# Performance work log

Measured on AMD Instinct MI355X. Metric: run time of the kernel, lower is better.

## Reference

```python
import jax, jax.numpy as jnp
import numpy as np

DIM = 1024
NUM_HEADS = 16
HEAD_DIM = DIM // NUM_HEADS
SCALE = HEAD_DIM ** -0.5


def rotate_half(x):
    x1, x2 = jnp.split(x, 2, axis=-1)
    return jnp.concatenate((-x2, x1), axis=-1)


def setup_inputs() -> dict:
    key = jax.random.key(0)
    ks = jax.random.split(key, 8)
    B, N = 2, 2048
    x = jax.random.normal(ks[0], (B, N, DIM), dtype=jnp.float32)
    # RoPE tables, broadcast over batch and heads
    pos = jnp.arange(N, dtype=jnp.float32)[:, None]
    inv_freq = 1.0 / (10000.0 ** (jnp.arange(0, HEAD_DIM, 2, dtype=jnp.float32) / HEAD_DIM))
    ang = pos * inv_freq[None, :]                       # [N, HEAD_DIM/2]
    ang = jnp.concatenate([ang, ang], axis=-1)          # [N, HEAD_DIM]
    rope_cos = jnp.cos(ang)[None, None]                 # [1,1,N,HEAD_DIM]
    rope_sin = jnp.sin(ang)[None, None]
    s = DIM ** -0.5
    qkv_w = jax.random.normal(ks[1], (3 * DIM, DIM), dtype=jnp.float32) * s
    qkv_b = jnp.zeros((3 * DIM,), dtype=jnp.float32)
    proj_w = jax.random.normal(ks[2], (DIM, DIM), dtype=jnp.float32) * s
    proj_b = jnp.zeros((DIM,), dtype=jnp.float32)
    return {"x": x, "rope_cos": rope_cos, "rope_sin": rope_sin,
            "qkv_w": qkv_w, "qkv_b": qkv_b, "proj_w": proj_w, "proj_b": proj_b}


def reference(x, rope_cos, rope_sin, qkv_w, qkv_b, proj_w, proj_b):
    B, N, C = x.shape
    H, D = NUM_HEADS, HEAD_DIM
    qkv = x @ qkv_w.T + qkv_b                            # [B,N,3C]
    qkv = qkv.reshape(B, N, 3, H, D).transpose(2, 0, 3, 1, 4)  # [3,B,H,N,D]
    q, k, v = qkv[0], qkv[1], qkv[2]
    # RoPE on q, k
    q = q * rope_cos + rotate_half(q) * rope_sin
    k = k * rope_cos + rotate_half(k) * rope_sin
    # scaled dot-product attention
    scores = jnp.einsum('bhnd,bhmd->bhnm', q, k) * SCALE
    attn = jax.nn.softmax(scores, axis=-1)
    out = jnp.einsum('bhnm,bhmd->bhnd', attn, v)         # [B,H,N,D]
    out = out.transpose(0, 2, 1, 3).reshape(B, N, C)
    return out @ proj_w.T + proj_b
```

## Files before the change

### kernel.cpp

```cpp
#include <hip/hip_runtime.h>
#include <hip/hip_bf16.h>

#define NUM_HEADS 16
#define HEAD_DIM 64
#define DIM 1024
#define NTOK 2048
#define MTOT 4096

typedef __attribute__((ext_vector_type(8))) short bf16x8;
typedef __attribute__((ext_vector_type(4))) float f32x4;
typedef __attribute__((ext_vector_type(16))) float f32x16;
typedef __attribute__((ext_vector_type(2))) unsigned int uint2v;

__device__ __forceinline__ unsigned short f2bf(float f) {
    union { __hip_bfloat16 h; unsigned short u; } c;
    c.h = __float2bfloat16(f);
    return c.u;
}

__device__ __forceinline__ unsigned int packbf(float lo, float hi) {
    union { unsigned short us[2]; unsigned int u; } p;
    p.us[0] = f2bf(lo); p.us[1] = f2bf(hi);
    return p.u;
}

__device__ __forceinline__ void plswap(unsigned int &a, unsigned int &b) {
#if __has_builtin(__builtin_amdgcn_permlane32_swap)
    uint2v r = __builtin_amdgcn_permlane32_swap(a, b, false, false);
    a = r[0]; b = r[1];
#else
    unsigned int pa = (unsigned int)__shfl_xor((int)a, 32);
    unsigned int pb = (unsigned int)__shfl_xor((int)b, 32);
    bool hi = (threadIdx.x & 32) != 0;
    unsigned int an = hi ? pb : a;
    unsigned int bn = hi ? b : pa;
    a = an; b = bn;
#endif
}

__device__ __forceinline__ void gload16(const unsigned short* g, unsigned short* l) {
    __builtin_amdgcn_global_load_lds(
        (const __attribute__((address_space(1))) void*)g,
        (__attribute__((address_space(3))) void*)l, 16, 0, 0);
}

__global__ __launch_bounds__(256) void k_conv3(
    const float* __restrict__ s0, unsigned short* __restrict__ d0, int n0,
    const float* __restrict__ s1, unsigned short* __restrict__ d1, int n1,
    const float* __restrict__ s2, unsigned short* __restrict__ d2, int n2)
{
    int blk = blockIdx.x;
    int b0 = n0 >> 11, b1 = n1 >> 11;
    const float* s; unsigned short* d; int i;
    if (blk < b0)            { s = s0; d = d0; i = blk; }
    else if (blk < b0 + b1)  { s = s1; d = d1; i = blk - b0; }
    else                     { s = s2; d = d2; i = blk - b0 - b1; }
    int idx = (i * 256 + threadIdx.x) * 8;
    float4 a = *(const float4*)(s + idx);
    float4 b = *(const float4*)(s + idx + 4);
    union { unsigned short us[8]; uint4 u4; } p;
    p.us[0] = f2bf(a.x); p.us[1] = f2bf(a.y); p.us[2] = f2bf(a.z); p.us[3] = f2bf(a.w);
    p.us[4] = f2bf(b.x); p.us[5] = f2bf(b.y); p.us[6] = f2bf(b.z); p.us[7] = f2bf(b.w);
    *(uint4*)(d + idx) = p.u4;
}

__global__ __launch_bounds__(256) void k_gemm_qkv(
    const unsigned short* __restrict__ xb, const unsigned short* __restrict__ wb,
    const float* __restrict__ bias, const float* __restrict__ rcos,
    const float* __restrict__ rsin,
    unsigned short* __restrict__ qb, unsigned short* __restrict__ kb,
    unsigned short* __restrict__ vtb)
{
    __shared__ __align__(16) unsigned char smem[34816];
    unsigned short* As = (unsigned short*)smem;
    unsigned short* Bs = (unsigned short*)(smem + 16384);

    const int tid  = threadIdx.x;
    const int lane = tid & 63;
    const int wid  = tid >> 6;
    const int lc   = lane & 31;
    const int hi   = lane >> 5;
    const int wm   = (wid >> 1) * 64;
    const int wn   = (wid & 1) * 64;
    const int m0   = blockIdx.y * 128;
    const int n0   = blockIdx.x * 128;

    const f32x16 z16 = {0.f,0.f,0.f,0.f, 0.f,0.f,0.f,0.f, 0.f,0.f,0.f,0.f, 0.f,0.f,0.f,0.f};
    f32x16 acc[2][2];
    acc[0][0] = z16; acc[0][1] = z16; acc[1][0] = z16; acc[1][1] = z16;

    for (int k0 = 0; k0 < DIM; k0 += 64) {
        #pragma unroll
        for (int it = 0; it < 4; ++it) {
            int p   = tid + it * 256;
            int row = p >> 3;
            int c   = (p & 7) ^ (row & 7);
            gload16(xb + (size_t)(m0 + row) * DIM + k0 + c*8, As + p*8);
            gload16(wb + (size_t)(n0 + row) * DIM + k0 + c*8, Bs + p*8);
        }
        __syncthreads();
        #pragma unroll
        for (int kk = 0; kk < 4; ++kk) {
            bf16x8 af[2], bfr[2];
            #pragma unroll
            for (int i = 0; i < 2; ++i) {
                int row = wm + i*32 + lc;
                af[i] = *(const bf16x8*)(As + row*64 + (((kk*2 + hi) ^ (row & 7)) << 3));
            }
            #pragma unroll
            for (int j = 0; j < 2; ++j) {
                int row = wn + j*32 + lc;
                bfr[j] = *(const bf16x8*)(Bs + row*64 + (((kk*2 + hi) ^ (row & 7)) << 3));
            }
            #pragma unroll
            for (int i = 0; i < 2; ++i)
                #pragma unroll
                for (int j = 0; j < 2; ++j)
                    acc[i][j] = __builtin_amdgcn_mfma_f32_32x32x16_bf16(af[i], bfr[j], acc[i][j], 0, 0, 0);
        }
        __syncthreads();
    }

    const int sect = n0 >> 10;
    float bq[2];
    #pragma unroll
    for (int j = 0; j < 2; ++j) bq[j] = bias[n0 + wn + j*32 + lc];

    if (sect < 2) {
        unsigned short* dst = sect ? kb : qb;
        const float sc = sect ? 1.0f : 0.125f * 1.44269504088896f;
        const int h = ((n0 & 1023) + wn) >> 6;
        #pragma unroll
        for (int i = 0; i < 2; ++i) {
            #pragma unroll
            for (int r = 0; r < 16; ++r) {
                int gm = m0 + wm + i*32 + (r & 3) + 8*(r >> 2) + 4*hi;
                int b  = gm >> 11, n = gm & 2047;
                size_t base = ((size_t)(b*NUM_HEADS + h) * NTOK + n) << 6;
                #pragma unroll
                for (int j = 0; j < 2; ++j) {
                    int d = j*32 + lc;
                    float val = acc[i][j][r] + bq[j];
                    float vp  = acc[i][j^1][r] + bq[j^1];
                    float rot = (j == 0) ? -vp : vp;
                    float c = rcos[n*64 + d], s = rsin[n*64 + d];
                    dst[base + d] = f2bf((val * c + rot * s) * sc);
                }
            }
        }
    } else {
        unsigned short (*vt)[136] = (unsigned short (*)[136])smem;
        __syncthreads();
        #pragma unroll
        for (int i = 0; i < 2; ++i)
            #pragma unroll
            for (int j = 0; j < 2; ++j)
                #pragma unroll
                for (int r = 0; r < 16; ++r) {
                    int row = wm + i*32 + (r & 3) + 8*(r >> 2) + 4*hi;
                    int c   = wn + j*32 + lc;
                    vt[c][row] = f2bf(acc[i][j][r] + bq[j]);
                }
        __syncthreads();
        const int b = m0 >> 11;
        const int nbase = m0 & 2047;
        #pragma unroll
        for (int it = 0; it < 8; ++it) {
            int c   = (tid >> 4) + it * 16;
            int sc2 = (n0 & 1023) + c;
            int hh  = sc2 >> 6, d = sc2 & 63;
            int nloc = (tid & 15) * 8;
            uint4 val = *(uint4*)&vt[c][nloc];
            *(uint4*)(vtb + ((size_t)(b*NUM_HEADS + hh) * HEAD_DIM + d) * NTOK + nbase + nloc) = val;
        }
    }
}

__global__ __launch_bounds__(256, 2) void k_attn(
    const unsigned short* __restrict__ qb, const unsigned short* __restrict__ kb,
    const unsigned short* __restrict__ vtb, unsigned short* __restrict__ attnb)
{
    __shared__ __align__(16) char sb[65536];

    const int tid  = threadIdx.x;
    const int lane = tid & 63;
    const int w    = tid >> 6;
    const int hi   = lane >> 5;
    const int lc   = lane & 31;
    const int qg   = w >> 1;
    const int kvg  = w & 1;
    const int q0   = blockIdx.y * 128;
    const int bh   = blockIdx.x;
    const int b    = bh >> 4, h = bh & 15;

    int koff[2][4];
    #pragma unroll
    for (int s = 0; s < 2; ++s)
        #pragma unroll
        for (int ks = 0; ks < 4; ++ks)
            koff[s][ks] = (64*kvg + 32*s + lc) * 128 + (((2*ks + hi) ^ (lc & 7)) << 4);
    int voff[2][4];
    #pragma unroll
    for (int dt = 0; dt < 2; ++dt)
        #pragma unroll
        for (int c4 = 0; c4 < 4; ++c4)
            voff[dt][c4] = 32768 + (32*dt + lc) * 256 + (((8*kvg + 2*c4 + hi) ^ (lc & 15)) << 4);

    const unsigned short* gk[4];
    const unsigned short* gv[4];
    char* dk[4]; char* dv[4];
    {
        const unsigned short* kbase = kb  + (size_t)bh * NTOK * 64;
        const unsigned short* vbase = vtb + (size_t)bh * HEAD_DIM * NTOK;
        #pragma unroll
        for (int it = 0; it < 4; ++it) {
            int p  = tid + it * 256;
            int kr = p >> 3;
            int kc = (p & 7) ^ (kr & 7);
            gk[it] = kbase + kr*64 + kc*8;
            dk[it] = sb + p*16;
            int vr = p >> 4;
            int vc = (p & 15) ^ (vr & 15);
            gv[it] = vbase + (size_t)vr*NTOK + vc*8;
            dv[it] = sb + 32768 + p*16;
        }
    }

    bf16x8 qa[2][4];
    #pragma unroll
    for (int qt = 0; qt < 2; ++qt) {
        size_t qrow = ((size_t)bh * NTOK + q0 + 64*qg + 32*qt + lc) * 64;
        #pragma unroll
        for (int ks = 0; ks < 4; ++ks)
            qa[qt][ks] = *(const bf16x8*)(qb + qrow + ks*16 + hi*8);
    }

    const f32x16 z16 = {0.f,0.f,0.f,0.f, 0.f,0.f,0.f,0.f, 0.f,0.f,0.f,0.f, 0.f,0.f,0.f,0.f};
    bf16x8 onesa;
    #pragma unroll
    for (int j = 0; j < 8; ++j) onesa[j] = (short)0x3F80;

    f32x16 o2[2][2];
    o2[0][0] = z16; o2[0][1] = z16; o2[1][0] = z16; o2[1][1] = z16;
    f32x16 ol0 = z16, ol1 = z16;

    #pragma unroll
    for (int it = 0; it < 4; ++it) {
        gload16(gk[it], (unsigned short*)dk[it]);
        gload16(gv[it], (unsigned short*)dv[it]);
        gk[it] += 8192; gv[it] += 128;
    }
    __syncthreads();

#define PACKQT(SS, PB0, PB1)                                                     \
    {                                                                            \
        _Pragma("unroll")                                                        \
        for (int u = 0; u < 2; ++u) {                                            \
            unsigned int a0 = packbf(SS[8*u],     SS[8*u + 1]);                  \
            unsigned int b0 = packbf(SS[8*u + 4], SS[8*u + 5]);                  \
            unsigned int a1 = packbf(SS[8*u + 2], SS[8*u + 3]);                  \
            unsigned int b1 = packbf(SS[8*u + 6], SS[8*u + 7]);                  \
            plswap(a0, b0);                                                      \
            plswap(a1, b1);                                                      \
            union { unsigned int u4[4]; bf16x8 v; } pk;                          \
            pk.u4[0] = a0; pk.u4[1] = a1; pk.u4[2] = b0; pk.u4[3] = b1;          \
            if (u == 0) (PB0) = pk.v; else (PB1) = pk.v;                         \
        }                                                                        \
    }

#define ATTN_ITER(X, DO_STAGE)                                                   \
    {                                                                            \
        if (DO_STAGE) {                                                          \
            _Pragma("unroll")                                                    \
            for (int it = 0; it < 4; ++it) {                                     \
                gload16(gk[it], (unsigned short*)(dk[it] + ((X) ^ 16384)));      \
                gload16(gv[it], (unsigned short*)(dv[it] + ((X) ^ 16384)));      \
                gk[it] += 8192; gv[it] += 128;                                   \
            }                                                                    \
        }                                                                        \
        _Pragma("unroll")                                                        \
        for (int s = 0; s < 2; ++s) {                                            \
            bf16x8 kf[4];                                                        \
            _Pragma("unroll")                                                    \
            for (int ks = 0; ks < 4; ++ks)                                       \
                kf[ks] = *(const bf16x8*)(sb + (X) + koff[s][ks]);               \
            __builtin_amdgcn_s_setprio(1);                                       \
            f32x16 S0 = __builtin_amdgcn_mfma_f32_32x32x16_bf16(kf[0], qa[0][0], z16, 0, 0, 0); \
            f32x16 S1 = __builtin_amdgcn_mfma_f32_32x32x16_bf16(kf[0], qa[1][0], z16, 0, 0, 0); \
            _Pragma("unroll")                                                    \
            for (int ks = 1; ks < 4; ++ks) {                                     \
                S0 = __builtin_amdgcn_mfma_f32_32x32x16_bf16(kf[ks], qa[0][ks], S0, 0, 0, 0); \
                S1 = __builtin_amdgcn_mfma_f32_32x32x16_bf16(kf[ks], qa[1][ks], S1, 0, 0, 0); \
            }                                                                    \
            __builtin_amdgcn_s_setprio(0);                                       \
            _Pragma("unroll")                                                    \
            for (int r = 0; r < 16; ++r) {                                       \
                S0[r] = __builtin_amdgcn_exp2f(S0[r]);                           \
                S1[r] = __builtin_amdgcn_exp2f(S1[r]);                           \
            }                                                                    \
            bf16x8 p00, p01, p10, p11;                                           \
            PACKQT(S0, p00, p01);                                                \
            PACKQT(S1, p10, p11);                                                \
            bf16x8 vf00 = *(const bf16x8*)(sb + (X) + voff[0][2*s + 0]);         \
            bf16x8 vf10 = *(const bf16x8*)(sb + (X) + voff[1][2*s + 0]);         \
            bf16x8 vf01 = *(const bf16x8*)(sb + (X) + voff[0][2*s + 1]);         \
            bf16x8 vf11 = *(const bf16x8*)(sb + (X) + voff[1][2*s + 1]);         \
            __builtin_amdgcn_s_setprio(1);                                       \
            o2[0][0] = __builtin_amdgcn_mfma_f32_32x32x16_bf16(vf00, p00, o2[0][0], 0, 0, 0); \
            o2[0][1] = __builtin_amdgcn_mfma_f32_32x32x16_bf16(vf10, p00, o2[0][1], 0, 0, 0); \
            o2[1][0] = __builtin_amdgcn_mfma_f32_32x32x16_bf16(vf00, p10, o2[1][0], 0, 0, 0); \
            o2[1][1] = __builtin_amdgcn_mfma_f32_32x32x16_bf16(vf10, p10, o2[1][1], 0, 0, 0); \
            o2[0][0] = __builtin_amdgcn_mfma_f32_32x32x16_bf16(vf01, p01, o2[0][0], 0, 0, 0); \
            o2[0][1] = __builtin_amdgcn_mfma_f32_32x32x16_bf16(vf11, p01, o2[0][1], 0, 0, 0); \
            o2[1][0] = __builtin_amdgcn_mfma_f32_32x32x16_bf16(vf01, p11, o2[1][0], 0, 0, 0); \
            o2[1][1] = __builtin_amdgcn_mfma_f32_32x32x16_bf16(vf11, p11, o2[1][1], 0, 0, 0); \
            ol0 = __builtin_amdgcn_mfma_f32_32x32x16_bf16(onesa, p00, ol0, 0, 0, 0); \
            ol0 = __builtin_amdgcn_mfma_f32_32x32x16_bf16(onesa, p01, ol0, 0, 0, 0); \
            ol1 = __builtin_amdgcn_mfma_f32_32x32x16_bf16(onesa, p10, ol1, 0, 0, 0); \
            ol1 = __builtin_amdgcn_mfma_f32_32x32x16_bf16(onesa, p11, ol1, 0, 0, 0); \
            __builtin_amdgcn_s_setprio(0);                                       \
        }                                                                        \
        __syncthreads();                                                         \
    }

    #pragma unroll 1
    for (int tt = 0; tt < NTOK/128; tt += 2) {
        ATTN_ITER(0,     true);
        ATTN_ITER(16384, (tt + 2 < NTOK/128));
    }
#undef ATTN_ITER
#undef PACKQT

    float lsum0 = ol0[0];
    float lsum1 = ol1[0];

    if (kvg == 1) {
        char* base = sb + qg * 16384;
        #pragma unroll
        for (int qt = 0; qt < 2; ++qt)
            #pragma unroll
            for (int dt = 0; dt < 2; ++dt)
                #pragma unroll
                for (int part = 0; part < 4; ++part) {
                    f32x4 v4;
                    #pragma unroll
                    for (int v = 0; v < 4; ++v) v4[v] = o2[qt][dt][part*4 + v];
                    *(f32x4*)(base + ((qt*2 + dt)*4 + part)*1024 + lane*16) = v4;
                }
        *(float*)(sb + 32768 + (qg*2 + 0)*256 + lane*4) = lsum0;
        *(float*)(sb + 32768 + (qg*2 + 1)*256 + lane*4) = lsum1;
    }
    __syncthreads();
    if (kvg == 0) {
        char* base = sb + qg * 16384;
        float lp0 = *(const float*)(sb + 32768 + (qg*2 + 0)*256 + lane*4);
        float lp1 = *(const float*)(sb + 32768 + (qg*2 + 1)*256 + lane*4);
        const float inv0 = 1.0f / (lsum0 + lp0);
        const float inv1 = 1.0f / (lsum1 + lp1);
        #pragma unroll
        for (int qt = 0; qt < 2; ++qt) {
            const float inv = qt ? inv1 : inv0;
            int q = q0 + 64*qg + 32*qt + lc;
            size_t obase = ((size_t)(b*NTOK + q)) * DIM + h*HEAD_DIM;
            #pragma unroll
            for (int dt = 0; dt < 2; ++dt)
                #pragma unroll
                for (int c = 0; c < 4; ++c) {
                    f32x4 vp = *(const f32x4*)(base + ((qt*2 + dt)*4 + c)*1024 + lane*16);
                    union { unsigned short us[4]; uint2 u2; } pk4;
                    #pragma unroll
                    for (int v = 0; v < 4; ++v)
                        pk4.us[v] = f2bf((o2[qt][dt][c*4 + v] + vp[v]) * inv);
                    *(uint2*)(attnb + obase + dt*32 + 8*c + 4*hi) = pk4.u2;
                }
        }
    }
}

__global__ __launch_bounds__(256) void k_proj(
    const unsigned short* __restrict__ a, const unsigned short* __restrict__ wb,
    const float* __restrict__ bias, float* __restrict__ out)
{
    __shared__ __align__(16) unsigned short As[8192];
    __shared__ __align__(16) unsigned short Bs[4096];

    const int tid  = threadIdx.x;
    const int lane = tid & 63;
    const int wid  = tid >> 6;
    const int lc   = lane & 31;
    const int hi   = lane >> 5;
    const int wm   = (wid & 1) * 64;
    const int wn   = (wid >> 1) * 32;
    const int m0   = blockIdx.y * 128;
    const int n0   = blockIdx.x * 64;

    const f32x16 z16 = {0.f,0.f,0.f,0.f, 0.f,0.f,0.f,0.f, 0.f,0.f,0.f,0.f, 0.f,0.f,0.f,0.f};
    f32x16 acc[2];
    acc[0] = z16; acc[1] = z16;

    for (int k0 = 0; k0 < DIM; k0 += 64) {
        #pragma unroll
        for (int it = 0; it < 4; ++it) {
            int p   = tid + it * 256;
            int row = p >> 3;
            int c   = (p & 7) ^ (row & 7);
            gload16(a + (size_t)(m0 + row) * DIM + k0 + c*8, As + p*8);
        }
        #pragma unroll
        for (int it = 0; it < 2; ++it) {
            int p   = tid + it * 256;
            int row = p >> 3;
            int c   = (p & 7) ^ (row & 7);
            gload16(wb + (size_t)(n0 + row) * DIM + k0 + c*8, Bs + p*8);
        }
        __syncthreads();
        #pragma unroll
        for (int kk = 0; kk < 4; ++kk) {
            bf16x8 af[2], bf;
            #pragma unroll
            for (int i = 0; i < 2; ++i) {
                int row = wm + i*32 + lc;
                af[i] = *(const bf16x8*)(As + row*64 + (((kk*2 + hi) ^ (row & 7)) << 3));
            }
            {
                int row = wn + lc;
                bf = *(const bf16x8*)(Bs + row*64 + (((kk*2 + hi) ^ (row & 7)) << 3));
            }
            #pragma unroll
            for (int i = 0; i < 2; ++i)
                acc[i] = __builtin_amdgcn_mfma_f32_32x32x16_bf16(af[i], bf, acc[i], 0, 0, 0);
        }
        __syncthreads();
    }

    #pragma unroll
    for (int i = 0; i < 2; ++i)
        #pragma unroll
        for (int r = 0; r < 16; ++r) {
            int row = m0 + wm + i*32 + (r & 3) + 8*(r >> 2) + 4*hi;
            int col = n0 + wn + lc;
            out[(size_t)row * DIM + col] = acc[i][r] + bias[col];
        }
}

extern "C" void kernel_launch(void* const* d_in, const int* in_sizes, int n_in,
                              void* d_out, int out_size, void* d_ws, size_t ws_size,
                              hipStream_t stream)
{
    const float* x      = (const float*)d_in[0];
    const float* rcos   = (const float*)d_in[1];
    const float* rsin   = (const float*)d_in[2];
    const float* qkv_w  = (const float*)d_in[3];
    const float* qkv_b  = (const float*)d_in[4];
    const float* proj_w = (const float*)d_in[5];
    const float* proj_b = (const float*)d_in[6];
    float* out = (float*)d_out;

    const size_t BUF = (size_t)2 * NUM_HEADS * NTOK * HEAD_DIM;
    unsigned short* qb    = (unsigned short*)d_ws;
    unsigned short* kb    = qb + BUF;
    unsigned short* vtb   = kb + BUF;
    unsigned short* attnb = vtb + BUF;
    unsigned short* xbf   = attnb + BUF;
    unsigned short* wqkvb = xbf + (size_t)MTOT * DIM;
    unsigned short* wprjb = wqkvb + (size_t)3 * DIM * DIM;

    const int n0 = MTOT * DIM, n1 = 3 * DIM * DIM, n2 = DIM * DIM;
    k_conv3<<<dim3((n0 + n1 + n2) / 2048), 256, 0, stream>>>(
        x, xbf, n0, qkv_w, wqkvb, n1, proj_w, wprjb, n2);

    k_gemm_qkv<<<dim3(24, 32), 256, 0, stream>>>(xbf, wqkvb, qkv_b, rcos, rsin, qb, kb, vtb);
    k_attn<<<dim3(32, NTOK/128), 256, 0, stream>>>(qb, kb, vtb, attnb);
    k_proj<<<dim3(16, 32), 256, 0, stream>>>(attnb, wprjb, proj_b, out);
}
```

Baseline: 117.3 us.

## Halve attention query tile, load V directly from global, and compute row sums in VALU

The attention kernel now handles 64 queries per block instead of 128 and uses half the shared memory, staging only K through LDS while V fragments are read straight from global memory each tile. The softmax denominator is accumulated with VALU adds and a cross-lane shuffle instead of extra MFMAs against a ones vector. Occupancy is raised to 4 blocks per CU. The aim is more parallelism and less LDS and MFMA overhead, but K/V reuse per block is halved and uncached global V loads may add latency.

Measured after the change: 225.8 us. 92.5% more time.

```diff
diff --git a/kernel.cpp b/kernel.cpp
--- a/kernel.cpp
+++ b/kernel.cpp
@@ -176,11 +176,11 @@
     }
 }
 
-__global__ __launch_bounds__(256, 2) void k_attn(
+__global__ __launch_bounds__(256, 4) void k_attn(
     const unsigned short* __restrict__ qb, const unsigned short* __restrict__ kb,
     const unsigned short* __restrict__ vtb, unsigned short* __restrict__ attnb)
 {
-    __shared__ __align__(16) char sb[65536];
+    __shared__ __align__(16) char sb[32768];
 
     const int tid  = threadIdx.x;
     const int lane = tid & 63;
@@ -189,29 +189,19 @@
     const int lc   = lane & 31;
     const int qg   = w >> 1;
     const int kvg  = w & 1;
-    const int q0   = blockIdx.y * 128;
+    const int q0   = blockIdx.y * 64;
     const int bh   = blockIdx.x;
     const int b    = bh >> 4, h = bh & 15;
 
-    int koff[2][4];
+    int koff4[4];
     #pragma unroll
-    for (int s = 0; s < 2; ++s)
-        #pragma unroll
-        for (int ks = 0; ks < 4; ++ks)
-            koff[s][ks] = (64*kvg + 32*s + lc) * 128 + (((2*ks + hi) ^ (lc & 7)) << 4);
-    int voff[2][4];
-    #pragma unroll
-    for (int dt = 0; dt < 2; ++dt)
-        #pragma unroll
-        for (int c4 = 0; c4 < 4; ++c4)
-            voff[dt][c4] = 32768 + (32*dt + lc) * 256 + (((8*kvg + 2*c4 + hi) ^ (lc & 15)) << 4);
+    for (int ks = 0; ks < 4; ++ks)
+        koff4[ks] = (64*kvg + lc) * 128 + (((2*ks + hi) ^ (lc & 7)) << 4);
 
     const unsigned short* gk[4];
-    const unsigned short* gv[4];
-    char* dk[4]; char* dv[4];
+    char* dk[4];
     {
-        const unsigned short* kbase = kb  + (size_t)bh * NTOK * 64;
-        const unsigned short* vbase = vtb + (size_t)bh * HEAD_DIM * NTOK;
+        const unsigned short* kbase = kb + (size_t)bh * NTOK * 64;
         #pragma unroll
         for (int it = 0; it < 4; ++it) {
             int p  = tid + it * 256;
@@ -219,38 +209,39 @@
             int kc = (p & 7) ^ (kr & 7);
             gk[it] = kbase + kr*64 + kc*8;
             dk[it] = sb + p*16;
-            int vr = p >> 4;
-            int vc = (p & 15) ^ (vr & 15);
-            gv[it] = vbase + (size_t)vr*NTOK + vc*8;
-            dv[it] = sb + 32768 + p*16;
-        }
-    }
-
-    bf16x8 qa[2][4];
-    #pragma unroll
-    for (int qt = 0; qt < 2; ++qt) {
-        size_t qrow = ((size_t)bh * NTOK + q0 + 64*qg + 32*qt + lc) * 64;
+        }
+    }
+
+    const unsigned short* vp0;
+    const unsigned short* vp1;
+    {
+        const unsigned short* vbase = vtb + (size_t)bh * HEAD_DIM * NTOK;
+        vp0 = vbase + (size_t)lc * NTOK + (8*kvg + hi)*8;
+        vp1 = vbase + (size_t)(32 + lc) * NTOK + (8*kvg + hi)*8;
+    }
+
+    bf16x8 qa[4];
+    {
+        size_t qrow = ((size_t)bh * NTOK + q0 + 32*qg + lc) * 64;
         #pragma unroll
         for (int ks = 0; ks < 4; ++ks)
-            qa[qt][ks] = *(const bf16x8*)(qb + qrow + ks*16 + hi*8);
+            qa[ks] = *(const bf16x8*)(qb + qrow + ks*16 + hi*8);
     }
 
     const f32x16 z16 = {0.f,0.f,0.f,0.f, 0.f,0.f,0.f,0.f, 0.f,0.f,0.f,0.f, 0.f,0.f,0.f,0.f};
-    bf16x8 onesa;
-    #pragma unroll
-    for (int j = 0; j < 8; ++j) onesa[j] = (short)0x3F80;
-
-    f32x16 o2[2][2];
-    o2[0][0] = z16; o2[0][1] = z16; o2[1][0] = z16; o2[1][1] = z16;
-    f32x16 ol0 = z16, ol1 = z16;
+    f32x16 o2[2];
+    o2[0] = z16; o2[1] = z16;
+    float lsum = 0.f;
 
     #pragma unroll
     for (int it = 0; it < 4; ++it) {
         gload16(gk[it], (unsigned short*)dk[it]);
-        gload16(gv[it], (unsigned short*)dv[it]);
-        gk[it] += 8192; gv[it] += 128;
+        gk[it] += 8192;
     }
     __syncthreads();
+
+#define SUM16(SS) ( (((SS[0]+SS[1])+(SS[2]+SS[3])) + ((SS[4]+SS[5])+(SS[6]+SS[7]))) + \
+                    (((SS[8]+SS[9])+(SS[10]+SS[11])) + ((SS[12]+SS[13])+(SS[14]+SS[15]))) )
 
 #define PACKQT(SS, PB0, PB1)                                                     \
     {                                                                            \
@@ -268,56 +259,45 @@
         }                                                                        \
     }
 
-#define ATTN_ITER(X, DO_STAGE)                                                   \
+#define ATTN_ITER(X, DO_STAGE, T)                                                \
     {                                                                            \
         if (DO_STAGE) {                                                          \
             _Pragma("unroll")                                                    \
             for (int it = 0; it < 4; ++it) {                                     \
                 gload16(gk[it], (unsigned short*)(dk[it] + ((X) ^ 16384)));      \
-                gload16(gv[it], (unsigned short*)(dv[it] + ((X) ^ 16384)));      \
-                gk[it] += 8192; gv[it] += 128;                                   \
+                gk[it] += 8192;                                                  \
             }                                                                    \
         }                                                                        \
+        const unsigned short* vt0 = vp0 + (T)*128;                               \
+        const unsigned short* vt1 = vp1 + (T)*128;                               \
         _Pragma("unroll")                                                        \
         for (int s = 0; s < 2; ++s) {                                            \
+                \
+            bf16x8 vf00 = *(const bf16x8*)(vt0 + (2*s + 0)*16);                  \
+            bf16x8 vf10 = *(const bf16x8*)(vt1 + (2*s + 0)*16);                  \
+            bf16x8 vf01 = *(const bf16x8*)(vt0 + (2*s + 1)*16);                  \
+            bf16x8 vf11 = *(const bf16x8*)(vt1 + (2*s + 1)*16);                  \
             bf16x8 kf[4];                                                        \
             _Pragma("unroll")                                                    \
             for (int ks = 0; ks < 4; ++ks)                                       \
-                kf[ks] = *(const bf16x8*)(sb + (X) + koff[s][ks]);               \
+                kf[ks] = *(const bf16x8*)(sb + (X) + s*4096 + koff4[ks]);        \
             __builtin_amdgcn_s_setprio(1);                                       \
-            f32x16 S0 = __builtin_amdgcn_mfma_f32_32x32x16_bf16(kf[0], qa[0][0], z16, 0, 0, 0); \
-            f32x16 S1 = __builtin_amdgcn_mfma_f32_32x32x16_bf16(kf[0], qa[1][0], z16, 0, 0, 0); \
+            f32x16 S = __builtin_amdgcn_mfma_f32_32x32x16_bf16(kf[0], qa[0], z16, 0, 0, 0); \
             _Pragma("unroll")                                                    \
-            for (int ks = 1; ks < 4; ++ks) {                                     \
-                S0 = __builtin_amdgcn_mfma_f32_32x32x16_bf16(kf[ks], qa[0][ks], S0, 0, 0, 0); \
-                S1 = __builtin_amdgcn_mfma_f32_32x32x16_bf16(kf[ks], qa[1][ks], S1, 0, 0, 0); \
-            }                                                                    \
+            for (int ks = 1; ks < 4; ++ks)                                       \
+                S = __builtin_amdgcn_mfma_f32_32x32x16_bf16(kf[ks], qa[ks], S, 0, 0, 0); \
             __builtin_amdgcn_s_setprio(0);                                       \
             _Pragma("unroll")                                                    \
-            for (int r = 0; r < 16; ++r) {                                       \
-                S0[r] = __builtin_amdgcn_exp2f(S0[r]);                           \
-                S1[r] = __builtin_amdgcn_exp2f(S1[r]);                           \
-            }                                                                    \
-            bf16x8 p00, p01, p10, p11;                                           \
-            PACKQT(S0, p00, p01);                                                \
-            PACKQT(S1, p10, p11);                                                \
-            bf16x8 vf00 = *(const bf16x8*)(sb + (X) + voff[0][2*s + 0]);         \
-            bf16x8 vf10 = *(const bf16x8*)(sb + (X) + voff[1][2*s + 0]);         \
-            bf16x8 vf01 = *(const bf16x8*)(sb + (X) + voff[0][2*s + 1]);         \
-            bf16x8 vf11 = *(const bf16x8*)(sb + (X) + voff[1][2*s + 1]);         \
+            for (int r = 0; r < 16; ++r)                                         \
+                S[r] = __builtin_amdgcn_exp2f(S[r]);                             \
+            lsum += SUM16(S);                                                    \
+            bf16x8 p0, p1;                                                       \
+            PACKQT(S, p0, p1);                                                   \
             __builtin_amdgcn_s_setprio(1);                                       \
-            o2[0][0] = __builtin_amdgcn_mfma_f32_32x32x16_bf16(vf00, p00, o2[0][0], 0, 0, 0); \
-            o2[0][1] = __builtin_amdgcn_mfma_f32_32x32x16_bf16(vf10, p00, o2[0][1], 0, 0, 0); \
-            o2[1][0] = __builtin_amdgcn_mfma_f32_32x32x16_bf16(vf00, p10, o2[1][0], 0, 0, 0); \
-            o2[1][1] = __builtin_amdgcn_mfma_f32_32x32x16_bf16(vf10, p10, o2[1][1], 0, 0, 0); \
-            o2[0][0] = __builtin_amdgcn_mfma_f32_32x32x16_bf16(vf01, p01, o2[0][0], 0, 0, 0); \
-            o2[0][1] = __builtin_amdgcn_mfma_f32_32x32x16_bf16(vf11, p01, o2[0][1], 0, 0, 0); \
-            o2[1][0] = __builtin_amdgcn_mfma_f32_32x32x16_bf16(vf01, p11, o2[1][0], 0, 0, 0); \
-            o2[1][1] = __builtin_amdgcn_mfma_f32_32x32x16_bf16(vf11, p11, o2[1][1], 0, 0, 0); \
-            ol0 = __builtin_amdgcn_mfma_f32_32x32x16_bf16(onesa, p00, ol0, 0, 0, 0); \
-            ol0 = __builtin_amdgcn_mfma_f32_32x32x16_bf16(onesa, p01, ol0, 0, 0, 0); \
-            ol1 = __builtin_amdgcn_mfma_f32_32x32x16_bf16(onesa, p10, ol1, 0, 0, 0); \
-            ol1 = __builtin_amdgcn_mfma_f32_32x32x16_bf16(onesa, p11, ol1, 0, 0, 0); \
+            o2[0] = __builtin_amdgcn_mfma_f32_32x32x16_bf16(vf00, p0, o2[0], 0, 0, 0); \
+            o2[1] = __builtin_amdgcn_mfma_f32_32x32x16_bf16(vf10, p0, o2[1], 0, 0, 0); \
+            o2[0] = __builtin_amdgcn_mfma_f32_32x32x16_bf16(vf01, p1, o2[0], 0, 0, 0); \
+            o2[1] = __builtin_amdgcn_mfma_f32_32x32x16_bf16(vf11, p1, o2[1], 0, 0, 0); \
             __builtin_amdgcn_s_setprio(0);                                       \
         }                                                                        \
         __syncthreads();                                                         \
@@ -325,55 +305,46 @@
 
     #pragma unroll 1
     for (int tt = 0; tt < NTOK/128; tt += 2) {
-        ATTN_ITER(0,     true);
-        ATTN_ITER(16384, (tt + 2 < NTOK/128));
+        ATTN_ITER(0,     true,                tt);
+        ATTN_ITER(16384, (tt + 2 < NTOK/128), tt + 1);
     }
 #undef ATTN_ITER
 #undef PACKQT
-
-    float lsum0 = ol0[0];
-    float lsum1 = ol1[0];
+#undef SUM16
+
+    lsum += __shfl_xor(lsum, 32);
 
     if (kvg == 1) {
-        char* base = sb + qg * 16384;
-        #pragma unroll
-        for (int qt = 0; qt < 2; ++qt)
-            #pragma unroll
-            for (int dt = 0; dt < 2; ++dt)
+        char* base = sb + qg * 8192;
+        #pragma unroll
+        for (int dt = 0; dt < 2; ++dt)
+            #pragma unroll
+            for (int part = 0; part < 4; ++part) {
+                f32x4 v4;
                 #pragma unroll
-                for (int part = 0; part < 4; ++part) {
-                    f32x4 v4;
-                    #pragma unroll
-                    for (int v = 0; v < 4; ++v) v4[v] = o2[qt][dt][part*4 + v];
-                    *(f32x4*)(base + ((qt*2 + dt)*4 + part)*1024 + lane*16) = v4;
-                }
-        *(float*)(sb + 32768 + (qg*2 + 0)*256 + lane*4) = lsum0;
-        *(float*)(sb + 32768 + (qg*2 + 1)*256 + lane*4) = lsum1;
+                for (int v = 0; v < 4; ++v) v4[v] = o2[dt][part*4 + v];
+                *(f32x4*)(base + (dt*4 + part)*1024 + lane*16) = v4;
+            }
+        *(float*)(sb + 16384 + qg*256 + lane*4) = lsum;
     }
     __syncthreads();
     if (kvg == 0) {
-        char* base = sb + qg * 16384;
-        float lp0 = *(const float*)(sb + 32768 + (qg*2 + 0)*256 + lane*4);
-        float lp1 = *(const float*)(sb + 32768 + (qg*2 + 1)*256 + lane*4);
-        const float inv0 = 1.0f / (lsum0 + lp0);
-        const float inv1 = 1.0f / (lsum1 + lp1);
-        #pragma unroll
-        for (int qt = 0; qt < 2; ++qt) {
-            const float inv = qt ? inv1 : inv0;
-            int q = q0 + 64*qg + 32*qt + lc;
-            size_t obase = ((size_t)(b*NTOK + q)) * DIM + h*HEAD_DIM;
-            #pragma unroll
-            for (int dt = 0; dt < 2; ++dt)
+        char* base = sb + qg * 8192;
+        float lp = *(const float*)(sb + 16384 + qg*256 + lane*4);
+        const float inv = 1.0f / (lsum + lp);
+        int q = q0 + 32*qg + lc;
+        size_t obase = ((size_t)(b*NTOK + q)) * DIM + h*HEAD_DIM;
+        #pragma unroll
+        for (int dt = 0; dt < 2; ++dt)
+            #pragma unroll
+            for (int c = 0; c < 4; ++c) {
+                f32x4 vp = *(const f32x4*)(base + (dt*4 + c)*1024 + lane*16);
+                union { unsigned short us[4]; uint2 u2; } pk4;
                 #pragma unroll
-                for (int c = 0; c < 4; ++c) {
-                    f32x4 vp = *(const f32x4*)(base + ((qt*2 + dt)*4 + c)*1024 + lane*16);
-                    union { unsigned short us[4]; uint2 u2; } pk4;
-                    #pragma unroll
-                    for (int v = 0; v < 4; ++v)
-                        pk4.us[v] = f2bf((o2[qt][dt][c*4 + v] + vp[v]) * inv);
-                    *(uint2*)(attnb + obase + dt*32 + 8*c + 4*hi) = pk4.u2;
-                }
-        }
+                for (int v = 0; v < 4; ++v)
+                    pk4.us[v] = f2bf((o2[dt][c*4 + v] + vp[v]) * inv);
+                *(uint2*)(attnb + obase + dt*32 + 8*c + 4*hi) = pk4.u2;
+            }
     }
 }
 
@@ -470,6 +441,6 @@
         x, xbf, n0, qkv_w, wqkvb, n1, proj_w, wprjb, n2);
 
     k_gemm_qkv<<<dim3(24, 32), 256, 0, stream>>>(xbf, wqkvb, qkv_b, rcos, rsin, qb, kb, vtb);
-    k_attn<<<dim3(32, NTOK/128), 256, 0, stream>>>(qb, kb, vtb, attnb);
+    k_attn<<<dim3(32, NTOK/64), 256, 0, stream>>>(qb, kb, vtb, attnb);
     k_proj<<<dim3(16, 32), 256, 0, stream>>>(attnb, wprjb, proj_b, out);
 }
```
